# Kernel tuning notes

Measured on AMD Instinct MI355X. Metric: run time of the kernel, lower is better.

## Reference

```python
import jax, jax.numpy as jnp
import numpy as np
import math

C = jnp.complex64
PI = math.pi
N = 4
D = 2 ** N  # 16

# ---- static single/two-qubit building blocks (numpy, complex64) ----
_I2 = np.eye(2, dtype=np.complex64)
_H = np.array([[1, 1], [1, -1]], dtype=np.complex64) / math.sqrt(2)

def _kron_list(ms):
    out = ms[0]
    for m in ms[1:]:
        out = np.kron(out, m)
    return out

# Hadamard expanded to qubit i of 4 (qubit 0 = most significant)
_HGATES = [jnp.asarray(_kron_list([_I2] * i + [_H] + [_I2] * (N - 1 - i))) for i in range(N)]

def _swap(i, j):
    idx = np.arange(D)
    bi = (idx >> (N - 1 - i)) & 1
    bj = (idx >> (N - 1 - j)) & 1
    d = bi ^ bj
    sw = idx ^ ((d << (N - 1 - i)) | (d << (N - 1 - j)))
    P = np.zeros((D, D), dtype=np.complex64)
    P[sw, idx] = 1.0
    return jnp.asarray(P)

_SW03 = _swap(0, 3)
_SW12 = _swap(1, 2)

# projectors on qubits 0,1 (4x4): |00><00|, |11><11|, |+><+|, |-><-| (Bell-like pair states)
_s0 = np.array([1, 0], dtype=np.complex64)
_s1 = np.array([0, 1], dtype=np.complex64)
_s00 = np.kron(_s0, _s0); _s11 = np.kron(_s1, _s1)
_sp = (np.kron(_s0, _s1) + np.kron(_s1, _s0)) / math.sqrt(2)
_sm = (np.kron(_s0, _s1) - np.kron(_s1, _s0)) / math.sqrt(2)
_P00 = jnp.asarray(np.outer(_s00, _s00.conj()))
_P11 = jnp.asarray(np.outer(_s11, _s11.conj()))
_Ppp = jnp.asarray(np.outer(_sp, _sp.conj()))
_Pmm = jnp.asarray(np.outer(_sm, _sm.conj()))
# Um = I4, so its term is a constant 16x16 matrix
_KMM = jnp.asarray(np.kron(np.outer(_sm, _sm.conj()), np.eye(4, dtype=np.complex64)))


def _blk(e, c0, c3):
    # [[c0,0,0,0],[0,a,b,0],[0,b,a,0],[0,0,0,c3]] with a=(e+1)/2, b=(e-1)/2
    one = jnp.ones((), C)
    z = jnp.zeros((), C)
    a = (e + one) * 0.5
    b = (e - one) * 0.5
    return jnp.stack([
        jnp.stack([c0, z, z, z]),
        jnp.stack([z, a, b, z]),
        jnp.stack([z, b, a, z]),
        jnp.stack([z, z, z, c3]),
    ])


def _U16(t):
    # t: float scalar. ep = e^{it}, em = e^{-it}
    ep = jax.lax.complex(jnp.cos(t), jnp.sin(t)).astype(C)
    em = jnp.conj(ep)
    one = jnp.ones((), C)
    U00 = _blk(em, one, em)
    U11 = _blk(ep, ep, one)
    z = jnp.zeros((), C)
    Up = jnp.diag(jnp.stack([ep, one, one, em]))
    return (jnp.kron(_P00, U00) + jnp.kron(_P11, U11)
            + jnp.kron(_Ppp, Up) + _KMM)


def _qft_U(thetas):
    oper = jnp.eye(D, dtype=C)
    n = 0
    for i in range(N):
        oper = _HGATES[i] @ oper
        for _ in range(i + 1, N):
            oper = _U16(thetas[n]) @ oper
            n += 1
    oper = _SW03 @ oper
    oper = _SW12 @ oper
    return oper


def setup_inputs() -> dict:
    key = jax.random.key(0)
    k1, k2, k3 = jax.random.split(key, 3)
    B, M = 8192, 128
    return {
        "inputs_re": jax.random.normal(k1, (B, D, M), dtype=jnp.float32),
        "inputs_im": jax.random.normal(k2, (B, D, M), dtype=jnp.float32),
        "thetas": jax.random.uniform(k3, (6,), dtype=jnp.float32, minval=0.0, maxval=2 * PI),
    }


def reference(inputs_re, inputs_im, thetas):
    inp = jax.lax.complex(inputs_re, inputs_im)  # [B,16,M] complex64
    gate = _qft_U(thetas)                        # [16,16] complex64
    # tf.matmul(qft_U, inputs) broadcast over batch
    return jnp.einsum("ij,bjm->bim", gate, inp)
```

## Files before the change

kernel.cpp:

```cpp
#include <hip/hip_runtime.h>


__device__ inline float hprod(int hq, int r, int c) {
    float v = 1.0f;
    for (int q = 0; q < 4; ++q) {
        int br = (r >> (3 - q)) & 1, bc = (c >> (3 - q)) & 1;
        if (q == hq) v *= 0.70710678118654752f * ((br & bc) ? -1.0f : 1.0f);
        else if (br != bc) return 0.0f;
    }
    return v;
}

__device__ inline float2 blk_e(float2 e, float2 c0, float2 c3, int i, int j) {
    float2 z = make_float2(0.f, 0.f);
    float2 a = make_float2((e.x + 1.f) * .5f, e.y * .5f);
    float2 b = make_float2((e.x - 1.f) * .5f, e.y * .5f);
    if (i == 0) return (j == 0) ? c0 : z;
    if (i == 3) return (j == 3) ? c3 : z;
    if (i == 1) return (j == 1) ? a : (j == 2 ? b : z);
      return (j == 2) ? a : (j == 1 ? b : z);
}

__device__ inline float2 u16_lit(int r, int c, float2 ep) {
    const float rt = 0.70710678118654752f;
    const float s00[4] = {1.f, 0.f, 0.f, 0.f};
    const float s11[4] = {0.f, 0.f, 0.f, 1.f};
    const float sp[4]  = {0.f,  rt,  rt, 0.f};
    const float sm[4]  = {0.f,  rt, -rt, 0.f};
    float2 em  = make_float2(ep.x, -ep.y);
    float2 one = make_float2(1.f, 0.f);
    int pr = r >> 2, qr = r & 3, pc = c >> 2, qc = c & 3;
    float2 acc = make_float2(0.f, 0.f);
    float p;
    p = s00[pr] * s00[pc];
    if (p != 0.f) { float2 u = blk_e(em, one, em, qr, qc); acc.x += p * u.x; acc.y += p * u.y; }
    p = s11[pr] * s11[pc];
    if (p != 0.f) { float2 u = blk_e(ep, ep, one, qr, qc); acc.x += p * u.x; acc.y += p * u.y; }
    p = sp[pr] * sp[pc];
    if (p != 0.f && qr == qc) {
        float2 u = (qr == 0) ? ep : (qr == 3 ? em : one);
        acc.x += p * u.x; acc.y += p * u.y;
    }
    p = sm[pr] * sm[pc];
    if (p != 0.f && qr == qc) acc.x += p;
    return acc;
}

__device__ inline int swrow(int r, int pi, int pj) {
    int bi = (r >> pi) & 1, bj = (r >> pj) & 1, d = bi ^ bj;
    return r ^ ((d << pi) | (d << pj));
}

__global__ void qft_gate_kernel(const float* __restrict__ thetas, float2* __restrict__ gate) {
    __shared__ float2 A[2][16][16];
    int t = threadIdx.x, i = t >> 4, j = t & 15;
    int cur = 0;
    A[0][i][j] = make_float2((i == j) ? 1.f : 0.f, 0.f);
    __syncthreads();
    const signed char kind [10] = {-1, 0, 0, 0, -1, 0, 0, -1, 0, -1};
    const signed char param[10] = { 0, 0, 1, 2,  1, 3, 4,  2, 5,  3};
    for (int s = 0; s < 10; ++s) {
        float2 acc = make_float2(0.f, 0.f);
        if (kind[s] < 0) {
            int hq = param[s];
            for (int k = 0; k < 16; ++k) {
                float g = hprod(hq, i, k);
                acc.x = fmaf(g, A[cur][k][j].x, acc.x);
                acc.y = fmaf(g, A[cur][k][j].y, acc.y);
            }
        } else {
            float th = thetas[(int)param[s]];
            float2 ep = make_float2(cosf(th), -sinf(th));
            for (int k = 0; k < 16; ++k) {
                float2 u = u16_lit(i, k, ep);
                float2 x = A[cur][k][j];
                acc.x += u.x * x.x - u.y * x.y;
                acc.y += u.x * x.y + u.y * x.x;
            }
        }
        A[cur ^ 1][i][j] = acc;
        cur ^= 1;
        __syncthreads();
    }
    A[cur ^ 1][i][j] = A[cur][swrow(i, 3, 0)][j];
    cur ^= 1; __syncthreads();
    A[cur ^ 1][i][j] = A[cur][swrow(i, 2, 1)][j];
    cur ^= 1; __syncthreads();
    gate[i * 16 + j] = A[cur][i][j];
}

__device__ inline unsigned int f2bf(float f) {
    unsigned int u = __float_as_uint(f);
    u += 0x7fffu + ((u >> 16) & 1u);
    return u >> 16;
}

__global__ __launch_bounds__(256) void qft_apply_kernel(
    const float* __restrict__ re, const float* __restrict__ im,
    const float2* __restrict__ gate, unsigned short* __restrict__ out)
{
    int b = blockIdx.x * 4 + (threadIdx.x >> 6);
    int lane = threadIdx.x & 63;

    const float2* pr = reinterpret_cast<const float2*>(re + b * 2048) + lane;
    const float2* pi = reinterpret_cast<const float2*>(im + b * 2048) + lane;

    float2 xr[16], xi[16];
#pragma unroll
    for (int j = 0; j < 16; ++j) {
        xr[j] = pr[j * 64];
        xi[j] = pi[j * 64];
    }

    unsigned short* po = out + (size_t)b * 4096 + lane * 4;
#pragma unroll
    for (int i = 0; i < 16; ++i) {
        float ar0 = 0.f, ai0 = 0.f, ar1 = 0.f, ai1 = 0.f;
#pragma unroll
        for (int j = 0; j < 16; ++j) {
            float2 g = gate[i * 16 + j];
            ar0 = fmaf(g.x, xr[j].x, ar0); ar0 = fmaf(-g.y, xi[j].x, ar0);
            ai0 = fmaf(g.y, xr[j].x, ai0); ai0 = fmaf(g.x, xi[j].x, ai0);
            ar1 = fmaf(g.x, xr[j].y, ar1); ar1 = fmaf(-g.y, xi[j].y, ar1);
            ai1 = fmaf(g.y, xr[j].y, ai1); ai1 = fmaf(g.x, xi[j].y, ai1);
        }
        uint2 w;
        w.x = f2bf(ar0) | (f2bf(ai0) << 16);
        w.y = f2bf(ar1) | (f2bf(ai1) << 16);
        *reinterpret_cast<uint2*>(po + (size_t)i * 256) = w;
    }
}

extern "C" void kernel_launch(void* const* d_in, const int* in_sizes, int n_in,
                              void* d_out, int out_size, void* d_ws, size_t ws_size,
                              hipStream_t stream) {
    const float* im = (const float*)d_in[0];
    const float* re = (const float*)d_in[1];
    const float* th = (const float*)d_in[2];
    float2* gate = (float2*)d_ws;
    unsigned short* out = (unsigned short*)d_out;

    qft_gate_kernel<<<1, 256, 0, stream>>>(th, gate);

    int B = in_sizes[0] / (16 * 128);
    qft_apply_kernel<<<B / 4, 256, 0, stream>>>(re, im, gate, out);
}
```

Measured before the change: 213.1 us.

## Fuse gate construction into apply kernel with sparse per-row gate stages

Removes the separate single-block gate-building kernel. Each apply block now rebuilds the 16x16 gate in shared memory using sparse two-term row updates for the Hadamard and U16 stages, folds the final swaps into a bit-reversed row index, and reads gate entries from LDS instead of global memory. This drops one launch and the serial dependency between the two kernels. In exchange every block repeats the small gate computation and its barriers, and occupancy is hinted via launch bounds.

```diff
diff --git a/kernel.cpp b/kernel.cpp
--- a/kernel.cpp
+++ b/kernel.cpp
@@ -1,93 +1,4 @@
 #include <hip/hip_runtime.h>
-
-
-__device__ inline float hprod(int hq, int r, int c) {
-    float v = 1.0f;
-    for (int q = 0; q < 4; ++q) {
-        int br = (r >> (3 - q)) & 1, bc = (c >> (3 - q)) & 1;
-        if (q == hq) v *= 0.70710678118654752f * ((br & bc) ? -1.0f : 1.0f);
-        else if (br != bc) return 0.0f;
-    }
-    return v;
-}
-
-__device__ inline float2 blk_e(float2 e, float2 c0, float2 c3, int i, int j) {
-    float2 z = make_float2(0.f, 0.f);
-    float2 a = make_float2((e.x + 1.f) * .5f, e.y * .5f);
-    float2 b = make_float2((e.x - 1.f) * .5f, e.y * .5f);
-    if (i == 0) return (j == 0) ? c0 : z;
-    if (i == 3) return (j == 3) ? c3 : z;
-    if (i == 1) return (j == 1) ? a : (j == 2 ? b : z);
-      return (j == 2) ? a : (j == 1 ? b : z);
-}
-
-__device__ inline float2 u16_lit(int r, int c, float2 ep) {
-    const float rt = 0.70710678118654752f;
-    const float s00[4] = {1.f, 0.f, 0.f, 0.f};
-    const float s11[4] = {0.f, 0.f, 0.f, 1.f};
-    const float sp[4]  = {0.f,  rt,  rt, 0.f};
-    const float sm[4]  = {0.f,  rt, -rt, 0.f};
-    float2 em  = make_float2(ep.x, -ep.y);
-    float2 one = make_float2(1.f, 0.f);
-    int pr = r >> 2, qr = r & 3, pc = c >> 2, qc = c & 3;
-    float2 acc = make_float2(0.f, 0.f);
-    float p;
-    p = s00[pr] * s00[pc];
-    if (p != 0.f) { float2 u = blk_e(em, one, em, qr, qc); acc.x += p * u.x; acc.y += p * u.y; }
-    p = s11[pr] * s11[pc];
-    if (p != 0.f) { float2 u = blk_e(ep, ep, one, qr, qc); acc.x += p * u.x; acc.y += p * u.y; }
-    p = sp[pr] * sp[pc];
-    if (p != 0.f && qr == qc) {
-        float2 u = (qr == 0) ? ep : (qr == 3 ? em : one);
-        acc.x += p * u.x; acc.y += p * u.y;
-    }
-    p = sm[pr] * sm[pc];
-    if (p != 0.f && qr == qc) acc.x += p;
-    return acc;
-}
-
-__device__ inline int swrow(int r, int pi, int pj) {
-    int bi = (r >> pi) & 1, bj = (r >> pj) & 1, d = bi ^ bj;
-    return r ^ ((d << pi) | (d << pj));
-}
-
-__global__ void qft_gate_kernel(const float* __restrict__ thetas, float2* __restrict__ gate) {
-    __shared__ float2 A[2][16][16];
-    int t = threadIdx.x, i = t >> 4, j = t & 15;
-    int cur = 0;
-    A[0][i][j] = make_float2((i == j) ? 1.f : 0.f, 0.f);
-    __syncthreads();
-    const signed char kind [10] = {-1, 0, 0, 0, -1, 0, 0, -1, 0, -1};
-    const signed char param[10] = { 0, 0, 1, 2,  1, 3, 4,  2, 5,  3};
-    for (int s = 0; s < 10; ++s) {
-        float2 acc = make_float2(0.f, 0.f);
-        if (kind[s] < 0) {
-            int hq = param[s];
-            for (int k = 0; k < 16; ++k) {
-                float g = hprod(hq, i, k);
-                acc.x = fmaf(g, A[cur][k][j].x, acc.x);
-                acc.y = fmaf(g, A[cur][k][j].y, acc.y);
-            }
-        } else {
-            float th = thetas[(int)param[s]];
-            float2 ep = make_float2(cosf(th), -sinf(th));
-            for (int k = 0; k < 16; ++k) {
-                float2 u = u16_lit(i, k, ep);
-                float2 x = A[cur][k][j];
-                acc.x += u.x * x.x - u.y * x.y;
-                acc.y += u.x * x.y + u.y * x.x;
-            }
-        }
-        A[cur ^ 1][i][j] = acc;
-        cur ^= 1;
-        __syncthreads();
-    }
-    A[cur ^ 1][i][j] = A[cur][swrow(i, 3, 0)][j];
-    cur ^= 1; __syncthreads();
-    A[cur ^ 1][i][j] = A[cur][swrow(i, 2, 1)][j];
-    cur ^= 1; __syncthreads();
-    gate[i * 16 + j] = A[cur][i][j];
-}
 
 __device__ inline unsigned int f2bf(float f) {
     unsigned int u = __float_as_uint(f);
@@ -95,30 +6,85 @@
     return u >> 16;
 }
 
-__global__ __launch_bounds__(256) void qft_apply_kernel(
+__device__ inline void u16_row(int r, float2 ep, int* c0, float2* v0, int* c1, float2* v1) {
+    float2 em   = make_float2(ep.x, -ep.y);
+    float2 one  = make_float2(1.f, 0.f);
+    float2 zero = make_float2(0.f, 0.f);
+    int pr = r >> 2, qr = r & 3;
+    if (pr == 0 || pr == 3) {
+        float2 e   = (pr == 0) ? em  : ep;
+        float2 cc0 = (pr == 0) ? one : ep;
+        float2 cc3 = (pr == 0) ? em  : one;
+        int base = (pr == 0) ? 0 : 12;
+        float2 a = make_float2((e.x + 1.f) * .5f, e.y * .5f);
+        float2 b = make_float2((e.x - 1.f) * .5f, e.y * .5f);
+        if      (qr == 0) { *c0 = base + 0; *v0 = cc0; *c1 = base + 0; *v1 = zero; }
+        else if (qr == 3) { *c0 = base + 3; *v0 = cc3; *c1 = base + 3; *v1 = zero; }
+        else if (qr == 1) { *c0 = base + 1; *v0 = a;   *c1 = base + 2; *v1 = b;    }
+        else              { *c0 = base + 1; *v0 = b;   *c1 = base + 2; *v1 = a;    }
+    } else {
+        float2 up = (qr == 0) ? ep : (qr == 3 ? em : one);
+        float hx = up.x * .5f, hy = up.y * .5f;
+        float s1 = (pr == 1) ? 0.5f : -0.5f;
+        float s2 = (pr == 2) ? 0.5f : -0.5f;
+        *c0 = 4 + qr; *v0 = make_float2(hx + s1, hy);
+        *c1 = 8 + qr; *v1 = make_float2(hx + s2, hy);
+    }
+}
+
+__global__ __launch_bounds__(256, 4) void qft_fused_kernel(
     const float* __restrict__ re, const float* __restrict__ im,
-    const float2* __restrict__ gate, unsigned short* __restrict__ out)
+    const float* __restrict__ thetas, unsigned short* __restrict__ out)
 {
-    int b = blockIdx.x * 4 + (threadIdx.x >> 6);
-    int lane = threadIdx.x & 63;
+    __shared__ float2 A[2][16][16];
+    int tid  = threadIdx.x;
+    int b    = blockIdx.x * 4 + (tid >> 6);
+    int lane = tid & 63;
+    int gi = tid >> 4, gj = tid & 15;
 
     const float2* pr = reinterpret_cast<const float2*>(re + b * 2048) + lane;
     const float2* pi = reinterpret_cast<const float2*>(im + b * 2048) + lane;
-
     float2 xr[16], xi[16];
 #pragma unroll
-    for (int j = 0; j < 16; ++j) {
-        xr[j] = pr[j * 64];
-        xi[j] = pi[j * 64];
+    for (int j = 0; j < 16; ++j) { xr[j] = pr[j * 64]; xi[j] = pi[j * 64]; }
+
+    A[0][gi][gj] = make_float2((gi == gj) ? 1.f : 0.f, 0.f);
+    __syncthreads();
+    const signed char kind [10] = {-1, 0, 0, 0, -1, 0, 0, -1, 0, -1};
+    const signed char param[10] = { 0, 0, 1, 2,  1, 3, 4,  2, 5,  3};
+#pragma unroll
+    for (int s = 0; s < 10; ++s) {
+        int src = s & 1, dst = src ^ 1;
+        float2 acc;
+        if (kind[s] < 0) {
+            int p  = 3 - param[s];
+            int i0 = gi & ~(1 << p), i1 = gi | (1 << p);
+            const float rt = 0.70710678118654752f;
+            float sg = ((gi >> p) & 1) ? -rt : rt;
+            float2 a0 = A[src][i0][gj], a1 = A[src][i1][gj];
+            acc.x = rt * a0.x + sg * a1.x;
+            acc.y = rt * a0.y + sg * a1.y;
+        } else {
+            float th = thetas[(int)param[s]];
+            float2 ep = make_float2(cosf(th), -sinf(th));
+            int c0, c1; float2 v0, v1;
+            u16_row(gi, ep, &c0, &v0, &c1, &v1);
+            float2 a0 = A[src][c0][gj], a1 = A[src][c1][gj];
+            acc.x = v0.x * a0.x - v0.y * a0.y + v1.x * a1.x - v1.y * a1.y;
+            acc.y = v0.x * a0.y + v0.y * a0.x + v1.x * a1.y + v1.y * a1.x;
+        }
+        A[dst][gi][gj] = acc;
+        __syncthreads();
     }
 
     unsigned short* po = out + (size_t)b * 4096 + lane * 4;
 #pragma unroll
     for (int i = 0; i < 16; ++i) {
+        const int rr = ((i & 1) << 3) | ((i & 2) << 1) | ((i & 4) >> 1) | ((i & 8) >> 3);
         float ar0 = 0.f, ai0 = 0.f, ar1 = 0.f, ai1 = 0.f;
 #pragma unroll
         for (int j = 0; j < 16; ++j) {
-            float2 g = gate[i * 16 + j];
+            float2 g = A[0][rr][j];
             ar0 = fmaf(g.x, xr[j].x, ar0); ar0 = fmaf(-g.y, xi[j].x, ar0);
             ai0 = fmaf(g.y, xr[j].x, ai0); ai0 = fmaf(g.x, xi[j].x, ai0);
             ar1 = fmaf(g.x, xr[j].y, ar1); ar1 = fmaf(-g.y, xi[j].y, ar1);
@@ -137,11 +103,8 @@
     const float* im = (const float*)d_in[0];
     const float* re = (const float*)d_in[1];
     const float* th = (const float*)d_in[2];
-    float2* gate = (float2*)d_ws;
     unsigned short* out = (unsigned short*)d_out;
 
-    qft_gate_kernel<<<1, 256, 0, stream>>>(th, gate);
-
     int B = in_sizes[0] / (16 * 128);
-    qft_apply_kernel<<<B / 4, 256, 0, stream>>>(re, im, gate, out);
+    qft_fused_kernel<<<B / 4, 256, 0, stream>>>(re, im, th, out);
 }
```

New measurement: 181.9 us. -14.6%, faster.
